# Kernel tuning notes

Measured on AMD Instinct MI355X. Metric: run time of the kernel, lower is better.

Reference implementation:

```python
import jax, jax.numpy as jnp
import numpy as np
import math

C_S, C_Z, C_H, H = 384, 128, 16, 12
B, N = 2, 512

def setup_inputs() -> dict:
    key = jax.random.key(0)
    ks = jax.random.split(key, 16)
    inp = {
        's': jax.random.normal(ks[0], (B, N, C_S), jnp.float32),
        'z': jax.random.normal(ks[1], (B, N, N, C_Z), jnp.float32),
        'translations': jax.random.normal(ks[2], (B, N, 3), jnp.float32) * 10.0,
        'rotations': jax.random.normal(ks[3], (B, N, 3, 3), jnp.float32),
        'mask': jnp.ones((B, N), dtype=bool),
        'Wq': jax.random.normal(ks[4], (C_S, H * C_H), jnp.float32) / math.sqrt(C_S),
        'bq': jnp.zeros((H * C_H,), jnp.float32),
        'Wk': jax.random.normal(ks[5], (C_S, H * C_H), jnp.float32) / math.sqrt(C_S),
        'bk': jnp.zeros((H * C_H,), jnp.float32),
        'Wv': jax.random.normal(ks[6], (C_S, H * C_H), jnp.float32) / math.sqrt(C_S),
        'bv': jnp.zeros((H * C_H,), jnp.float32),
        'Wb': jax.random.normal(ks[7], (C_Z, H), jnp.float32) / math.sqrt(C_Z),
        'bb': jnp.zeros((H,), jnp.float32),
        'Wout': jax.random.normal(ks[8], (H * (C_H + C_Z), C_S), jnp.float32) / math.sqrt(H * (C_H + C_Z)),
        'bout': jnp.zeros((C_S,), jnp.float32),
    }
    return inp


def _multiscale_bias(coords):
    # pairwise euclidean distance (B, N, N)
    diff = coords[:, :, None, :] - coords[:, None, :, :]
    d = jnp.sqrt(jnp.sum(diff * diff, axis=-1))
    bias = jnp.where(d <= 5.0, 1.0, jnp.where(d <= 15.0, 0.3, 0.05))
    return bias[..., None]  # (B, N, N, 1)


def reference(s, z, translations, rotations, mask, Wq, bq, Wk, bk, Wv, bv, Wb, bb, Wout, bout):
    b, n, _ = s.shape
    q = (s @ Wq + bq).reshape(b, n, H, C_H)
    k = (s @ Wk + bk).reshape(b, n, H, C_H)
    v = (s @ Wv + bv).reshape(b, n, H, C_H)
    attn = jnp.einsum('bihc,bjhc->bijh', q, k) / math.sqrt(C_H)
    attn = attn + (z @ Wb + bb) + _multiscale_bias(translations)
    m2 = mask[:, None, :] & mask[:, :, None]  # (B, N_i, N_j)
    attn = jnp.where(m2[..., None], attn, -1e9)
    w = jax.nn.softmax(attn, axis=2)  # softmax over j
    scalar = jnp.einsum('bijh,bjhc->bihc', w, v)
    pair = jnp.einsum('bijh,bijc->bihc', w, z)
    out = jnp.concatenate([scalar, pair], axis=-1).reshape(b, n, -1)
    return out @ Wout + bout
```

## Files before the change

kernel.cpp:

```cpp
#include <hip/hip_runtime.h>

#define H_    12
#define CH_   16
#define CZ_   128
#define CS_   384
#define N_    512
#define QKV_  192
#define CXF_  1728
#define TJ_   64
#define NT_   (N_ / TJ_)

typedef __attribute__((ext_vector_type(8))) short short8_t;
typedef __attribute__((ext_vector_type(4))) float f32x4;
typedef __attribute__((ext_vector_type(4))) unsigned u32x4;

__device__ inline unsigned bf16pack(float a, float b) {
    unsigned ua = __builtin_bit_cast(unsigned, a);
    unsigned ub = __builtin_bit_cast(unsigned, b);
    unsigned lo = (ua + 0x7fffu + ((ua >> 16) & 1u)) >> 16;
    unsigned hi = (ub + 0x7fffu + ((ub >> 16) & 1u)) & 0xffff0000u;
    return lo | hi;
}
__device__ inline unsigned short bf16one(float a) {
    unsigned ua = __builtin_bit_cast(unsigned, a);
    return (unsigned short)((ua + 0x7fffu + ((ua >> 16) & 1u)) >> 16);
}
__device__ inline float bfl(unsigned u) { return __builtin_bit_cast(float, u << 16); }
__device__ inline float bfh(unsigned u) { return __builtin_bit_cast(float, u & 0xffff0000u); }

#define ZIDX(c, j) ((c) * 72 + ((j) ^ ((((c) >> 2) & 7) << 3)))

__global__ __launch_bounds__(192) void qkv_kernel(
    const float* __restrict__ s,
    const float* __restrict__ Wq, const float* __restrict__ bq,
    const float* __restrict__ Wk, const float* __restrict__ bk,
    const float* __restrict__ Wv, const float* __restrict__ bv,
    float* __restrict__ Q, float* __restrict__ Ko, unsigned short* __restrict__ Vt)
{
    __shared__ float s_s[4][CS_];
    const int t = threadIdx.x;
    const int row0 = blockIdx.x * 4;
    for (int idx = t; idx < 4 * CS_; idx += 192) {
        int r = idx / CS_, c = idx - r * CS_;
        s_s[r][c] = s[(size_t)(row0 + r) * CS_ + c];
    }
    __syncthreads();
    float aq[4], ak[4], av[4];
    const float bqv = bq[t], bkv = bk[t], bvv = bv[t];
    #pragma unroll
    for (int r = 0; r < 4; ++r) { aq[r] = bqv; ak[r] = bkv; av[r] = bvv; }
    for (int c = 0; c < CS_; ++c) {
        float wq = Wq[c * QKV_ + t];
        float wk = Wk[c * QKV_ + t];
        float wv = Wv[c * QKV_ + t];
        #pragma unroll
        for (int r = 0; r < 4; ++r) {
            float sv = s_s[r][c];
            aq[r] = fmaf(sv, wq, aq[r]);
            ak[r] = fmaf(sv, wk, ak[r]);
            av[r] = fmaf(sv, wv, av[r]);
        }
    }
    #pragma unroll
    for (int r = 0; r < 4; ++r) {
        Q [(size_t)(row0 + r) * QKV_ + t] = aq[r];
        Ko[(size_t)(row0 + r) * QKV_ + t] = ak[r];
        Vt[(size_t)t * (2 * N_) + row0 + r] = bf16one(av[r]);
    }
}

__global__ __launch_bounds__(256, 5) void attn_kernel(
    const float* __restrict__ z, const float* __restrict__ trans,
    const float* __restrict__ Wb, const float* __restrict__ bb,
    const float* __restrict__ Q, const float* __restrict__ Kv,
    const unsigned short* __restrict__ Vt, float* __restrict__ X)
{
    __shared__ unsigned short z16s[CZ_ * 72];
    __shared__ float l_s[16][72];
    __shared__ float q_s[H_ * 20];
    __shared__ float dist_s[TJ_];
    __shared__ float bb_s[16];
    __shared__ float alpha_s[16];
    __shared__ float sum_s[16];
    __shared__ float ti_s[3];

    const int t = threadIdx.x;
    const int bi = blockIdx.x;
    const int b = bi >> 9, i = bi & (N_ - 1);
    const size_t zrow = (size_t)(b * N_ + i) * N_ * CZ_;
    const int wave = t >> 6, lane = t & 63;
    const int g   = (lane >> 4) & 3;
    const int hx  = lane & 15;

    for (int p = t; p < 4 * 72; p += 256) l_s[12 + p / 72][p % 72] = 0.f;
    if (t < QKV_) q_s[(t >> 4) * 20 + (t & 15)] = Q[(size_t)(b * N_ + i) * QKV_ + t];
    if (t < 16) {
        bb_s[t] = (t < H_) ? bb[t] : 0.f;
        alpha_s[t] = 1.f;
    }
    if (t < 3) ti_s[t] = trans[(size_t)(b * N_ + i) * 3 + t];

    short8_t wbf0, wbf1, wbf2, wbf3;
    {
        u32x4 wv;
        #pragma unroll
        for (int kk = 0; kk < 4; ++kk) {
            #pragma unroll
            for (int p2 = 0; p2 < 4; ++p2) {
                int c0 = kk * 32 + g * 8 + 2 * p2;
                float w0 = (hx < H_) ? Wb[c0 * H_ + hx] : 0.f;
                float w1 = (hx < H_) ? Wb[(c0 + 1) * H_ + hx] : 0.f;
                wv[p2] = bf16pack(w0, w1);
            }
            if (kk == 0) wbf0 = __builtin_bit_cast(short8_t, wv);
            else if (kk == 1) wbf1 = __builtin_bit_cast(short8_t, wv);
            else if (kk == 2) wbf2 = __builtin_bit_cast(short8_t, wv);
            else wbf3 = __builtin_bit_cast(short8_t, wv);
        }
    }

    float acc_sc = 0.f;
    float m_run = -1e30f, sum_run = 0.f;
    f32x4 accP0 = (f32x4){0.f, 0.f, 0.f, 0.f};
    f32x4 accP1 = (f32x4){0.f, 0.f, 0.f, 0.f};

    for (int tile = 0; tile < NT_; ++tile) {
        const int j0 = tile * TJ_;
        __syncthreads();

        {
            const float* zt = z + zrow + (size_t)j0 * CZ_;
            #pragma unroll
            for (int it = 0; it < 4; ++it) {
                int idx = it * 256 + t;
                int c4 = idx & 31;
                int jj = (idx >> 5) * 2;
                float4 a0 = *((const float4*)(zt + (size_t)jj * CZ_) + c4);
                float4 a1 = *((const float4*)(zt + (size_t)(jj + 1) * CZ_) + c4);
                int jb = jj ^ ((c4 & 7) << 3);
                *(unsigned*)&z16s[(c4 * 4 + 0) * 72 + jb] = bf16pack(a0.x, a1.x);
                *(unsigned*)&z16s[(c4 * 4 + 1) * 72 + jb] = bf16pack(a0.y, a1.y);
                *(unsigned*)&z16s[(c4 * 4 + 2) * 72 + jb] = bf16pack(a0.z, a1.z);
                *(unsigned*)&z16s[(c4 * 4 + 3) * 72 + jb] = bf16pack(a0.w, a1.w);
            }
        }

        #pragma unroll
        for (int r = 0; r < 3; ++r) {
            int p = r * 256 + t;
            int j = p / 12, h = p - 12 * j;
            const float4* kg = reinterpret_cast<const float4*>(
                Kv + ((size_t)(b * N_ + j0 + j) * QKV_ + h * 16));
            const float4* qg = reinterpret_cast<const float4*>(q_s + h * 20);
            float4 k0 = kg[0], k1 = kg[1], k2 = kg[2], k3 = kg[3];
            float4 q0 = qg[0], q1 = qg[1], q2 = qg[2], q3 = qg[3];
            float acc;
            acc  = k0.x*q0.x + k0.y*q0.y + k0.z*q0.z + k0.w*q0.w;
            acc += k1.x*q1.x + k1.y*q1.y + k1.z*q1.z + k1.w*q1.w;
            acc += k2.x*q2.x + k2.y*q2.y + k2.z*q2.z + k2.w*q2.w;
            acc += k3.x*q3.x + k3.y*q3.y + k3.z*q3.z + k3.w*q3.w;
            l_s[h][j] = acc * 0.25f;
        }

        if (t < TJ_) {
            size_t tj = (size_t)(b * N_ + j0 + t) * 3;
            float dx = trans[tj + 0] - ti_s[0];
            float dy = trans[tj + 1] - ti_s[1];
            float dz = trans[tj + 2] - ti_s[2];
            float d2 = dx * dx + dy * dy + dz * dz;
            dist_s[t] = d2 <= 25.f ? 1.f : (d2 <= 225.f ? 0.3f : 0.05f);
        }
        __syncthreads();

        {
            const int jA = wave * 16 + hx;
            f32x4 accB = (f32x4){0.f, 0.f, 0.f, 0.f};
            #pragma unroll
            for (int kk = 0; kk < 4; ++kk) {
                const int cb = kk * 32 + g * 8;
                u32x4 af;
                #pragma unroll
                for (int p2 = 0; p2 < 4; ++p2) {
                    unsigned lo = z16s[ZIDX(cb + 2 * p2,     jA)];
                    unsigned hi = z16s[ZIDX(cb + 2 * p2 + 1, jA)];
                    af[p2] = lo | (hi << 16);
                }
                short8_t av = __builtin_bit_cast(short8_t, af);
                accB = __builtin_amdgcn_mfma_f32_16x16x32_bf16(
                    av, (kk == 0 ? wbf0 : kk == 1 ? wbf1 : kk == 2 ? wbf2 : wbf3),
                    accB, 0, 0, 0);
            }
            if (hx < H_) {
                #pragma unroll
                for (int reg = 0; reg < 4; ++reg) {
                    int j = wave * 16 + g * 4 + reg;
                    l_s[hx][j] += accB[reg] + bb_s[hx] + dist_s[j];
                }
            }
        }
        __syncthreads();

        if (wave < 3) {
            const int h = wave * 4 + g;
            float4 v = *(const float4*)&l_s[h][hx * 4];
            float mt = fmaxf(fmaxf(v.x, v.y), fmaxf(v.z, v.w));
            #pragma unroll
            for (int off = 1; off < 16; off <<= 1)
                mt = fmaxf(mt, __shfl_xor(mt, off));
            float mn = fmaxf(m_run, mt);
            float al = __expf(m_run - mn);
            m_run = mn;
            float4 e;
            e.x = __expf(v.x - mn); e.y = __expf(v.y - mn);
            e.z = __expf(v.z - mn); e.w = __expf(v.w - mn);
            *(float4*)&l_s[h][hx * 4] = e;
            float st = e.x + e.y + e.z + e.w;
            #pragma unroll
            for (int off = 1; off < 16; off <<= 1)
                st += __shfl_xor(st, off);
            sum_run = sum_run * al + st;
            if (hx == 0) alpha_s[h] = al;
            __asm__ volatile("s_waitcnt lgkmcnt(0)" ::: "memory");
            const unsigned short* vt = Vt + (size_t)t * (2 * N_) + (b * N_ + j0);
            float a = 0.f;
            #pragma unroll
            for (int q8 = 0; q8 < 8; ++q8) {
                u32x4 uv = *(const u32x4*)(vt + q8 * 8);
                float4 w0 = *(const float4*)&l_s[h][q8 * 8];
                float4 w1 = *(const float4*)&l_s[h][q8 * 8 + 4];
                a = fmaf(bfl(uv[0]), w0.x, a); a = fmaf(bfh(uv[0]), w0.y, a);
                a = fmaf(bfl(uv[1]), w0.z, a); a = fmaf(bfh(uv[1]), w0.w, a);
                a = fmaf(bfl(uv[2]), w1.x, a); a = fmaf(bfh(uv[2]), w1.y, a);
                a = fmaf(bfl(uv[3]), w1.z, a); a = fmaf(bfh(uv[3]), w1.w, a);
            }
            acc_sc = acc_sc * al + a;
        }
        __syncthreads();

        {
            short8_t aw0, aw1;
            {
                u32x4 p;
                #pragma unroll
                for (int kk = 0; kk < 2; ++kk) {
                    const float4 x0 = *(const float4*)&l_s[hx][kk * 32 + g * 8];
                    const float4 x1 = *(const float4*)&l_s[hx][kk * 32 + g * 8 + 4];
                    p[0] = bf16pack(x0.x, x0.y); p[1] = bf16pack(x0.z, x0.w);
                    p[2] = bf16pack(x1.x, x1.y); p[3] = bf16pack(x1.z, x1.w);
                    if (kk == 0) aw0 = __builtin_bit_cast(short8_t, p);
                    else         aw1 = __builtin_bit_cast(short8_t, p);
                }
            }
            const float a0 = alpha_s[g * 4 + 0], a1 = alpha_s[g * 4 + 1];
            const float a2 = alpha_s[g * 4 + 2], a3 = alpha_s[g * 4 + 3];
            {
                const int cB = (wave * 2 + 0) * 16 + hx;
                accP0[0] *= a0; accP0[1] *= a1; accP0[2] *= a2; accP0[3] *= a3;
                short8_t bz0 = *(const short8_t*)&z16s[ZIDX(cB, g * 8)];
                short8_t bz1 = *(const short8_t*)&z16s[ZIDX(cB, 32 + g * 8)];
                accP0 = __builtin_amdgcn_mfma_f32_16x16x32_bf16(aw0, bz0, accP0, 0, 0, 0);
                accP0 = __builtin_amdgcn_mfma_f32_16x16x32_bf16(aw1, bz1, accP0, 0, 0, 0);
            }
            {
                const int cB = (wave * 2 + 1) * 16 + hx;
                accP1[0] *= a0; accP1[1] *= a1; accP1[2] *= a2; accP1[3] *= a3;
                short8_t bz0 = *(const short8_t*)&z16s[ZIDX(cB, g * 8)];
                short8_t bz1 = *(const short8_t*)&z16s[ZIDX(cB, 32 + g * 8)];
                accP1 = __builtin_amdgcn_mfma_f32_16x16x32_bf16(aw0, bz0, accP1, 0, 0, 0);
                accP1 = __builtin_amdgcn_mfma_f32_16x16x32_bf16(aw1, bz1, accP1, 0, 0, 0);
            }
        }
    }

    if (wave < 3 && hx == 0) sum_s[wave * 4 + g] = sum_run;
    __syncthreads();

    const size_t xbase = (size_t)(b * N_ + i) * CXF_;
    if (t < QKV_) {
        int h = t >> 4, c = t & 15;
        X[xbase + h * 144 + c] = acc_sc / sum_run;
    }
    {
        const int cB0 = (wave * 2 + 0) * 16 + hx;
        const int cB1 = (wave * 2 + 1) * 16 + hx;
        #pragma unroll
        for (int reg = 0; reg < 4; ++reg) {
            int h = g * 4 + reg;
            if (h < H_) {
                float inv = 1.f / sum_s[h];
                X[xbase + (size_t)h * 144 + 16 + cB0] = accP0[reg] * inv;
                X[xbase + (size_t)h * 144 + 16 + cB1] = accP1[reg] * inv;
            }
        }
    }
}

__global__ __launch_bounds__(256) void outproj_kernel(
    const float* __restrict__ X, const float* __restrict__ Wout,
    const float* __restrict__ bout, float* __restrict__ out)
{
    __shared__ float Xs[32][36];
    __shared__ float Ws[32][68];
    const int t = threadIdx.x;
    const int row0 = blockIdx.x * 32;
    const int col0 = blockIdx.y * 64;
    const int rg = t >> 4, cg = t & 15;
    float acc[2][4] = {};
    for (int k0 = 0; k0 < CXF_; k0 += 32) {
        __syncthreads();
        {
            int r = t >> 3, k4 = t & 7;
            float4 v4 = *reinterpret_cast<const float4*>(
                X + (size_t)(row0 + r) * CXF_ + k0 + k4 * 4);
            *reinterpret_cast<float4*>(&Xs[r][k4 * 4]) = v4;
        }
        {
            int kr = t >> 4, cc4 = t & 15;
            *reinterpret_cast<float4*>(&Ws[kr][cc4 * 4]) =
                *reinterpret_cast<const float4*>(Wout + (size_t)(k0 + kr) * CS_ + col0 + cc4 * 4);
            *reinterpret_cast<float4*>(&Ws[kr + 16][cc4 * 4]) =
                *reinterpret_cast<const float4*>(Wout + (size_t)(k0 + kr + 16) * CS_ + col0 + cc4 * 4);
        }
        __syncthreads();
        #pragma unroll
        for (int kk = 0; kk < 32; ++kk) {
            float a0 = Xs[rg * 2 + 0][kk];
            float a1 = Xs[rg * 2 + 1][kk];
            float4 w4 = *reinterpret_cast<const float4*>(&Ws[kk][cg * 4]);
            acc[0][0] = fmaf(a0, w4.x, acc[0][0]);
            acc[0][1] = fmaf(a0, w4.y, acc[0][1]);
            acc[0][2] = fmaf(a0, w4.z, acc[0][2]);
            acc[0][3] = fmaf(a0, w4.w, acc[0][3]);
            acc[1][0] = fmaf(a1, w4.x, acc[1][0]);
            acc[1][1] = fmaf(a1, w4.y, acc[1][1]);
            acc[1][2] = fmaf(a1, w4.z, acc[1][2]);
            acc[1][3] = fmaf(a1, w4.w, acc[1][3]);
        }
    }
    #pragma unroll
    for (int rr = 0; rr < 2; ++rr) {
        int row = row0 + rg * 2 + rr;
        #pragma unroll
        for (int u = 0; u < 4; ++u) {
            int col = col0 + cg * 4 + u;
            out[(size_t)row * CS_ + col] = acc[rr][u] + bout[col];
        }
    }
}

extern "C" void kernel_launch(void* const* d_in, const int* in_sizes, int n_in,
                              void* d_out, int out_size, void* d_ws, size_t ws_size,
                              hipStream_t stream)
{
    const float* s     = (const float*)d_in[0];
    const float* z     = (const float*)d_in[1];
    const float* trans = (const float*)d_in[2];
    const float* Wq    = (const float*)d_in[5];
    const float* bq    = (const float*)d_in[6];
    const float* Wk    = (const float*)d_in[7];
    const float* bk    = (const float*)d_in[8];
    const float* Wv    = (const float*)d_in[9];
    const float* bv    = (const float*)d_in[10];
    const float* Wb    = (const float*)d_in[11];
    const float* bbp   = (const float*)d_in[12];
    const float* Wout  = (const float*)d_in[13];
    const float* bout  = (const float*)d_in[14];
    float* out = (float*)d_out;

    float* ws = (float*)d_ws;
    float* Q  = ws;
    float* K  = ws + 196608;
    unsigned short* Vt = (unsigned short*)(ws + 393216);
    float* X  = ws + 491520;

    qkv_kernel<<<256, 192, 0, stream>>>(s, Wq, bq, Wk, bk, Wv, bv, Q, K, Vt);
    attn_kernel<<<1024, 256, 0, stream>>>(z, trans, Wb, bbp, Q, K, Vt, X);
    dim3 gridC(32, 6);
    outproj_kernel<<<gridC, 256, 0, stream>>>(X, Wout, bout, out);
}
```

Before: 260.4 us.

## Prefetch z tiles into registers, precompute logits upfront, use fp32 V, shrink outproj tiles

The attention kernel now loads the next z tile into registers while the current one is processed, and computes all QK logits plus the distance and bias terms for every tile before the main loop. This is meant to hide global-load latency behind MFMA work. V is stored in fp32 instead of bf16, which doubles V traffic but removes the unpack work. The occupancy hint drops from 5 to 4 to make room for the extra registers. The output projection uses 16-row tiles to launch twice as many blocks.

```diff
diff --git a/kernel.cpp b/kernel.cpp
--- a/kernel.cpp
+++ b/kernel.cpp
@@ -14,19 +14,13 @@
 typedef __attribute__((ext_vector_type(4))) float f32x4;
 typedef __attribute__((ext_vector_type(4))) unsigned u32x4;
 
-__device__ inline unsigned bf16pack(float a, float b) {
+__device__ inline unsigned bfpk(float a, float b) {
     unsigned ua = __builtin_bit_cast(unsigned, a);
     unsigned ub = __builtin_bit_cast(unsigned, b);
     unsigned lo = (ua + 0x7fffu + ((ua >> 16) & 1u)) >> 16;
     unsigned hi = (ub + 0x7fffu + ((ub >> 16) & 1u)) & 0xffff0000u;
     return lo | hi;
 }
-__device__ inline unsigned short bf16one(float a) {
-    unsigned ua = __builtin_bit_cast(unsigned, a);
-    return (unsigned short)((ua + 0x7fffu + ((ua >> 16) & 1u)) >> 16);
-}
-__device__ inline float bfl(unsigned u) { return __builtin_bit_cast(float, u << 16); }
-__device__ inline float bfh(unsigned u) { return __builtin_bit_cast(float, u & 0xffff0000u); }
 
 #define ZIDX(c, j) ((c) * 72 + ((j) ^ ((((c) >> 2) & 7) << 3)))
 
@@ -35,7 +29,7 @@
     const float* __restrict__ Wq, const float* __restrict__ bq,
     const float* __restrict__ Wk, const float* __restrict__ bk,
     const float* __restrict__ Wv, const float* __restrict__ bv,
-    float* __restrict__ Q, float* __restrict__ Ko, unsigned short* __restrict__ Vt)
+    float* __restrict__ Q, float* __restrict__ Ko, float* __restrict__ Vt)
 {
     __shared__ float s_s[4][CS_];
     const int t = threadIdx.x;
@@ -65,29 +59,28 @@
     for (int r = 0; r < 4; ++r) {
         Q [(size_t)(row0 + r) * QKV_ + t] = aq[r];
         Ko[(size_t)(row0 + r) * QKV_ + t] = ak[r];
-        Vt[(size_t)t * (2 * N_) + row0 + r] = bf16one(av[r]);
-    }
-}
-
-__global__ __launch_bounds__(256, 5) void attn_kernel(
+        Vt[(size_t)t * (2 * N_) + row0 + r] = av[r];
+    }
+}
+
+__global__ __launch_bounds__(256, 4) void attn_kernel(
     const float* __restrict__ z, const float* __restrict__ trans,
     const float* __restrict__ Wb, const float* __restrict__ bb,
     const float* __restrict__ Q, const float* __restrict__ Kv,
-    const unsigned short* __restrict__ Vt, float* __restrict__ X)
+    const float* __restrict__ Vt, float* __restrict__ X)
 {
     __shared__ unsigned short z16s[CZ_ * 72];
     __shared__ float l_s[16][72];
     __shared__ float q_s[H_ * 20];
-    __shared__ float dist_s[TJ_];
     __shared__ float bb_s[16];
     __shared__ float alpha_s[16];
     __shared__ float sum_s[16];
-    __shared__ float ti_s[3];
 
     const int t = threadIdx.x;
     const int bi = blockIdx.x;
     const int b = bi >> 9, i = bi & (N_ - 1);
     const size_t zrow = (size_t)(b * N_ + i) * N_ * CZ_;
+    const float* zt = z + zrow;
     const int wave = t >> 6, lane = t & 63;
     const int g   = (lane >> 4) & 3;
     const int hx  = lane & 15;
@@ -98,7 +91,42 @@
         bb_s[t] = (t < H_) ? bb[t] : 0.f;
         alpha_s[t] = 1.f;
     }
-    if (t < 3) ti_s[t] = trans[(size_t)(b * N_ + i) * 3 + t];
+    __syncthreads();
+
+    float4 zA[4], zB[4];
+    #pragma unroll
+    for (int it = 0; it < 4; ++it) {
+        int idx = it * 256 + t;
+        int c4 = idx & 31, jj = (idx >> 5) * 2;
+        zA[it] = *((const float4*)(zt + (size_t)jj * CZ_) + c4);
+        zB[it] = *((const float4*)(zt + (size_t)(jj + 1) * CZ_) + c4);
+    }
+
+    const float ti0 = trans[(size_t)(b * N_ + i) * 3 + 0];
+    const float ti1 = trans[(size_t)(b * N_ + i) * 3 + 1];
+    const float ti2 = trans[(size_t)(b * N_ + i) * 3 + 2];
+    float lg[24];
+    #pragma unroll
+    for (int u = 0; u < 24; ++u) {
+        const int tl = u / 3, r = u - 3 * tl;
+        const int p = r * 256 + t;
+        const int jl = p / 12, h = p - 12 * jl;
+        const int jg = tl * TJ_ + jl;
+        const float4* kg = (const float4*)(Kv + (size_t)(b * N_ + jg) * QKV_ + h * 16);
+        const float4* qg = (const float4*)(q_s + h * 20);
+        float4 k0 = kg[0], k1 = kg[1], k2 = kg[2], k3 = kg[3];
+        float4 q0 = qg[0], q1 = qg[1], q2 = qg[2], q3 = qg[3];
+        float acc;
+        acc  = k0.x*q0.x + k0.y*q0.y + k0.z*q0.z + k0.w*q0.w;
+        acc += k1.x*q1.x + k1.y*q1.y + k1.z*q1.z + k1.w*q1.w;
+        acc += k2.x*q2.x + k2.y*q2.y + k2.z*q2.z + k2.w*q2.w;
+        acc += k3.x*q3.x + k3.y*q3.y + k3.z*q3.z + k3.w*q3.w;
+        const float* tp = trans + (size_t)(b * N_ + jg) * 3;
+        float dx = tp[0] - ti0, dy = tp[1] - ti1, dz = tp[2] - ti2;
+        float d2 = dx * dx + dy * dy + dz * dz;
+        float bias = d2 <= 25.f ? 1.f : (d2 <= 225.f ? 0.3f : 0.05f);
+        lg[u] = acc * 0.25f + bb_s[h] + bias;
+    }
 
     short8_t wbf0, wbf1, wbf2, wbf3;
     {
@@ -110,7 +138,7 @@
                 int c0 = kk * 32 + g * 8 + 2 * p2;
                 float w0 = (hx < H_) ? Wb[c0 * H_ + hx] : 0.f;
                 float w1 = (hx < H_) ? Wb[(c0 + 1) * H_ + hx] : 0.f;
-                wv[p2] = bf16pack(w0, w1);
+                wv[p2] = bfpk(w0, w1);
             }
             if (kk == 0) wbf0 = __builtin_bit_cast(short8_t, wv);
             else if (kk == 1) wbf1 = __builtin_bit_cast(short8_t, wv);
@@ -124,51 +152,35 @@
     f32x4 accP0 = (f32x4){0.f, 0.f, 0.f, 0.f};
     f32x4 accP1 = (f32x4){0.f, 0.f, 0.f, 0.f};
 
+    #pragma unroll
     for (int tile = 0; tile < NT_; ++tile) {
         const int j0 = tile * TJ_;
         __syncthreads();
 
-        {
-            const float* zt = z + zrow + (size_t)j0 * CZ_;
+        #pragma unroll
+        for (int it = 0; it < 4; ++it) {
+            int idx = it * 256 + t;
+            int c4 = idx & 31, jj = (idx >> 5) * 2;
+            int jb = jj ^ ((c4 & 7) << 3);
+            *(unsigned*)&z16s[(c4 * 4 + 0) * 72 + jb] = bfpk(zA[it].x, zB[it].x);
+            *(unsigned*)&z16s[(c4 * 4 + 1) * 72 + jb] = bfpk(zA[it].y, zB[it].y);
+            *(unsigned*)&z16s[(c4 * 4 + 2) * 72 + jb] = bfpk(zA[it].z, zB[it].z);
+            *(unsigned*)&z16s[(c4 * 4 + 3) * 72 + jb] = bfpk(zA[it].w, zB[it].w);
+        }
+        #pragma unroll
+        for (int r = 0; r < 3; ++r) {
+            int p = r * 256 + t;
+            int jl = p / 12, h = p - 12 * jl;
+            l_s[h][jl] = lg[tile * 3 + r];
+        }
+        if (tile + 1 < NT_) {
             #pragma unroll
             for (int it = 0; it < 4; ++it) {
                 int idx = it * 256 + t;
-                int c4 = idx & 31;
-                int jj = (idx >> 5) * 2;
-                float4 a0 = *((const float4*)(zt + (size_t)jj * CZ_) + c4);
-                float4 a1 = *((const float4*)(zt + (size_t)(jj + 1) * CZ_) + c4);
-                int jb = jj ^ ((c4 & 7) << 3);
-                *(unsigned*)&z16s[(c4 * 4 + 0) * 72 + jb] = bf16pack(a0.x, a1.x);
-                *(unsigned*)&z16s[(c4 * 4 + 1) * 72 + jb] = bf16pack(a0.y, a1.y);
-                *(unsigned*)&z16s[(c4 * 4 + 2) * 72 + jb] = bf16pack(a0.z, a1.z);
-                *(unsigned*)&z16s[(c4 * 4 + 3) * 72 + jb] = bf16pack(a0.w, a1.w);
-            }
-        }
-
-        #pragma unroll
-        for (int r = 0; r < 3; ++r) {
-            int p = r * 256 + t;
-            int j = p / 12, h = p - 12 * j;
-            const float4* kg = reinterpret_cast<const float4*>(
-                Kv + ((size_t)(b * N_ + j0 + j) * QKV_ + h * 16));
-            const float4* qg = reinterpret_cast<const float4*>(q_s + h * 20);
-            float4 k0 = kg[0], k1 = kg[1], k2 = kg[2], k3 = kg[3];
-            float4 q0 = qg[0], q1 = qg[1], q2 = qg[2], q3 = qg[3];
-            float acc;
-            acc  = k0.x*q0.x + k0.y*q0.y + k0.z*q0.z + k0.w*q0.w;
-            acc += k1.x*q1.x + k1.y*q1.y + k1.z*q1.z + k1.w*q1.w;
-            acc += k2.x*q2.x + k2.y*q2.y + k2.z*q2.z + k2.w*q2.w;
-            acc += k3.x*q3.x + k3.y*q3.y + k3.z*q3.z + k3.w*q3.w;
-            l_s[h][j] = acc * 0.25f;
-        }
-
-        if (t < TJ_) {
-            size_t tj = (size_t)(b * N_ + j0 + t) * 3;
-            float dx = trans[tj + 0] - ti_s[0];
-            float dy = trans[tj + 1] - ti_s[1];
-            float dz = trans[tj + 2] - ti_s[2];
-            float d2 = dx * dx + dy * dy + dz * dz;
-            dist_s[t] = d2 <= 25.f ? 1.f : (d2 <= 225.f ? 0.3f : 0.05f);
+                int c4 = idx & 31, jj = (idx >> 5) * 2;
+                zA[it] = *((const float4*)(zt + (size_t)(j0 + TJ_ + jj) * CZ_) + c4);
+                zB[it] = *((const float4*)(zt + (size_t)(j0 + TJ_ + jj + 1) * CZ_) + c4);
+            }
         }
         __syncthreads();
 
@@ -194,7 +206,7 @@
                 #pragma unroll
                 for (int reg = 0; reg < 4; ++reg) {
                     int j = wave * 16 + g * 4 + reg;
-                    l_s[hx][j] += accB[reg] + bb_s[hx] + dist_s[j];
+                    l_s[hx][j] += accB[reg];
                 }
             }
         }
@@ -221,17 +233,17 @@
             sum_run = sum_run * al + st;
             if (hx == 0) alpha_s[h] = al;
             __asm__ volatile("s_waitcnt lgkmcnt(0)" ::: "memory");
-            const unsigned short* vt = Vt + (size_t)t * (2 * N_) + (b * N_ + j0);
+            __builtin_amdgcn_sched_barrier(0);
+            const float4* vp = (const float4*)(Vt + (size_t)t * (2 * N_) + (b * N_ + j0));
             float a = 0.f;
             #pragma unroll
-            for (int q8 = 0; q8 < 8; ++q8) {
-                u32x4 uv = *(const u32x4*)(vt + q8 * 8);
-                float4 w0 = *(const float4*)&l_s[h][q8 * 8];
-                float4 w1 = *(const float4*)&l_s[h][q8 * 8 + 4];
-                a = fmaf(bfl(uv[0]), w0.x, a); a = fmaf(bfh(uv[0]), w0.y, a);
-                a = fmaf(bfl(uv[1]), w0.z, a); a = fmaf(bfh(uv[1]), w0.w, a);
-                a = fmaf(bfl(uv[2]), w1.x, a); a = fmaf(bfh(uv[2]), w1.y, a);
-                a = fmaf(bfl(uv[3]), w1.z, a); a = fmaf(bfh(uv[3]), w1.w, a);
+            for (int q4 = 0; q4 < 16; ++q4) {
+                float4 vv = vp[q4];
+                float4 ww = *(const float4*)&l_s[h][q4 * 4];
+                a = fmaf(vv.x, ww.x, a);
+                a = fmaf(vv.y, ww.y, a);
+                a = fmaf(vv.z, ww.z, a);
+                a = fmaf(vv.w, ww.w, a);
             }
             acc_sc = acc_sc * al + a;
         }
@@ -245,8 +257,8 @@
                 for (int kk = 0; kk < 2; ++kk) {
                     const float4 x0 = *(const float4*)&l_s[hx][kk * 32 + g * 8];
                     const float4 x1 = *(const float4*)&l_s[hx][kk * 32 + g * 8 + 4];
-                    p[0] = bf16pack(x0.x, x0.y); p[1] = bf16pack(x0.z, x0.w);
-                    p[2] = bf16pack(x1.x, x1.y); p[3] = bf16pack(x1.z, x1.w);
+                    p[0] = bfpk(x0.x, x0.y); p[1] = bfpk(x0.z, x0.w);
+                    p[2] = bfpk(x1.x, x1.y); p[3] = bfpk(x1.z, x1.w);
                     if (kk == 0) aw0 = __builtin_bit_cast(short8_t, p);
                     else         aw1 = __builtin_bit_cast(short8_t, p);
                 }
@@ -299,16 +311,16 @@
     const float* __restrict__ X, const float* __restrict__ Wout,
     const float* __restrict__ bout, float* __restrict__ out)
 {
-    __shared__ float Xs[32][36];
+    __shared__ float Xs[16][36];
     __shared__ float Ws[32][68];
     const int t = threadIdx.x;
-    const int row0 = blockIdx.x * 32;
+    const int row0 = blockIdx.x * 16;
     const int col0 = blockIdx.y * 64;
     const int rg = t >> 4, cg = t & 15;
-    float acc[2][4] = {};
+    float acc[4] = {};
     for (int k0 = 0; k0 < CXF_; k0 += 32) {
         __syncthreads();
-        {
+        if (t < 128) {
             int r = t >> 3, k4 = t & 7;
             float4 v4 = *reinterpret_cast<const float4*>(
                 X + (size_t)(row0 + r) * CXF_ + k0 + k4 * 4);
@@ -324,26 +336,20 @@
         __syncthreads();
         #pragma unroll
         for (int kk = 0; kk < 32; ++kk) {
-            float a0 = Xs[rg * 2 + 0][kk];
-            float a1 = Xs[rg * 2 + 1][kk];
+            float a0 = Xs[rg][kk];
             float4 w4 = *reinterpret_cast<const float4*>(&Ws[kk][cg * 4]);
-            acc[0][0] = fmaf(a0, w4.x, acc[0][0]);
-            acc[0][1] = fmaf(a0, w4.y, acc[0][1]);
-            acc[0][2] = fmaf(a0, w4.z, acc[0][2]);
-            acc[0][3] = fmaf(a0, w4.w, acc[0][3]);
-            acc[1][0] = fmaf(a1, w4.x, acc[1][0]);
-            acc[1][1] = fmaf(a1, w4.y, acc[1][1]);
-            acc[1][2] = fmaf(a1, w4.z, acc[1][2]);
-            acc[1][3] = fmaf(a1, w4.w, acc[1][3]);
-        }
-    }
-    #pragma unroll
-    for (int rr = 0; rr < 2; ++rr) {
-        int row = row0 + rg * 2 + rr;
+            acc[0] = fmaf(a0, w4.x, acc[0]);
+            acc[1] = fmaf(a0, w4.y, acc[1]);
+            acc[2] = fmaf(a0, w4.z, acc[2]);
+            acc[3] = fmaf(a0, w4.w, acc[3]);
+        }
+    }
+    {
+        int row = row0 + rg;
         #pragma unroll
         for (int u = 0; u < 4; ++u) {
             int col = col0 + cg * 4 + u;
-            out[(size_t)row * CS_ + col] = acc[rr][u] + bout[col];
+            out[(size_t)row * CS_ + col] = acc[u] + bout[col];
         }
     }
 }
@@ -370,11 +376,11 @@
     float* ws = (float*)d_ws;
     float* Q  = ws;
     float* K  = ws + 196608;
-    unsigned short* Vt = (unsigned short*)(ws + 393216);
-    float* X  = ws + 491520;
+    float* Vt = ws + 393216;
+    float* X  = ws + 589824;
 
     qkv_kernel<<<256, 192, 0, stream>>>(s, Wq, bq, Wk, bk, Wv, bv, Q, K, Vt);
     attn_kernel<<<1024, 256, 0, stream>>>(z, trans, Wb, bbp, Q, K, Vt, X);
-    dim3 gridC(32, 6);
+    dim3 gridC(64, 6);
     outproj_kernel<<<gridC, 256, 0, stream>>>(X, Wout, bout, out);
 }
```

After: 531.9 us. 2.04x slower.
